# Optimization experiments

Hardware: AMD Instinct MI355X
Metric: run time of the kernel (lower is better)

## Reference

```python
import jax, jax.numpy as jnp
import numpy as np

TOP_K = 2
TEMP = 1.0  # router_temperature
B, L, D, F, DF, DR, DH, E = 32, 256, 256, 8, 64, 256, 512, 8
DIN = D + DF  # expert/router input: concat(hidden, feat_emb)


def setup_inputs() -> dict:
    key = jax.random.key(0)
    ks = jax.random.split(key, 12)
    gn = lambda k, shape, fan: jax.random.normal(k, shape, dtype=jnp.float32) * (fan ** -0.5)
    return {
        "hidden": jax.random.normal(ks[0], (B, L, D), dtype=jnp.float32),
        "feat": jax.random.uniform(ks[1], (B, L, F), dtype=jnp.float32),
        "W_feat": gn(ks[2], (F, DF), F),
        "b_feat": jnp.zeros((DF,), jnp.float32),
        "Wr1": gn(ks[3], (DIN, DR), DIN),
        "br1": jnp.zeros((DR,), jnp.float32),
        "Wr2": gn(ks[4], (DR, E), DR),
        "br2": jnp.zeros((E,), jnp.float32),
        "We1": gn(ks[5], (E, DIN, DH), DIN),
        "be1": jnp.zeros((E, DH), jnp.float32),
        "We2": gn(ks[6], (E, DH, D), DH),
        "be2": jnp.zeros((E, D), jnp.float32),
    }


def reference(hidden, feat, W_feat, b_feat, Wr1, br1, Wr2, br2, We1, be1, We2, be2):
    # feature embedding
    feat_emb = feat @ W_feat + b_feat                       # [B,L,DF]
    x = jnp.concatenate([hidden, feat_emb], axis=-1)        # [B,L,DIN]

    # token-level learned router with temperature + top-k gating
    hr = jax.nn.gelu(x @ Wr1 + br1)                         # [B,L,DR]
    gate_logits = (hr @ Wr2 + br2) / TEMP                   # [B,L,E]
    topv, topi = jax.lax.top_k(gate_logits, TOP_K)          # [B,L,K]
    w = jax.nn.softmax(topv, axis=-1)                       # renormalized over top-k
    gate_weights = (jax.nn.one_hot(topi, E, dtype=w.dtype) * w[..., None]).sum(-2)  # [B,L,E]

    # experts: per-expert 2-layer MLP (dense compute, sparse combine via gates)
    he = jax.nn.gelu(jnp.einsum('bli,eih->bleh', x, We1) + be1)   # [B,L,E,DH]
    eo = jnp.einsum('bleh,eho->bleo', he, We2) + be2              # [B,L,E,D]
    stage_delta = jnp.einsum('ble,bleo->blo', gate_weights, eo)   # next_hidden - hidden

    return stage_delta, gate_weights, gate_logits
```

## Files before the change

### kernel.cpp

```cpp
#include <hip/hip_runtime.h>
#include <hip/hip_bf16.h>

#define N_TOK   8192
#define DMODEL  256
#define NFEAT   8
#define DFEAT   64
#define DIN     320
#define DRTR    256
#define NE      8
#define DH      512
#define TE      32
#define RTB     32
#define FIXCAP  128
#define FIXTHR  2e-3f

#define OUT_GATEW  (N_TOK*DMODEL)
#define OUT_LOGITS (N_TOK*DMODEL + N_TOK*NE)

typedef short v8s __attribute__((ext_vector_type(8)));
typedef float v4f __attribute__((ext_vector_type(4)));

__device__ __forceinline__ unsigned short f2bf(float f){
  unsigned u = __float_as_uint(f);
  return (unsigned short)((u + 0x7FFFu + ((u>>16)&1u)) >> 16);
}
__device__ __forceinline__ float bf2f(unsigned short h){
  return __uint_as_float(((unsigned)h)<<16);
}
__device__ __forceinline__ float gelu_tanh(float v){
  float u = 0.7978845608028654f * (v + 0.044715f * v * v * v);
  float a = fabsf(u);
  float e = __expf(-2.0f * a);
  float t = (1.0f - e) / (1.0f + e);
  t = copysignf(t, u);
  return 0.5f * v * (1.0f + t);
}

__global__ __launch_bounds__(256) void k_prep(
    const float* __restrict__ We1, const float* __restrict__ We2,
    const float* __restrict__ Wr1,
    unsigned short* __restrict__ W1h, unsigned short* __restrict__ W1l,
    unsigned short* __restrict__ W2h, unsigned short* __restrict__ W2l,
    unsigned short* __restrict__ Wr1h, unsigned short* __restrict__ Wr1l,
    int* __restrict__ cnts, int* __restrict__ nfix)
{
  __shared__ float lds[16384];
  const int b = blockIdx.x;
  const int tid = threadIdx.x;
  if (b < 80){
    int e = b/10, kstep = b%10;
    const float* src = We1 + ((size_t)e*DIN + kstep*32)*DH;
    #pragma unroll
    for (int r=0;r<16;r++) ((float4*)lds)[r*256+tid] = ((const float4*)src)[r*256+tid];
    __syncthreads();
    #pragma unroll
    for (int r=0;r<8;r++){
      int ent = r*256+tid; int nt = ent>>6, l = ent&63;
      int n = nt*16 + (l&15); int k0 = (l>>4)*8;
      unsigned short hs[8], ls[8];
      #pragma unroll
      for (int i=0;i<8;i++){
        float v = lds[(k0+i)*DH + n];
        unsigned short h = f2bf(v);
        hs[i]=h; ls[i]=f2bf(v - bf2f(h));
      }
      size_t gid = ((size_t)(e*10+kstep)*32 + nt)*64 + l;
      *(v8s*)(W1h+gid*8) = *(v8s*)hs;
      *(v8s*)(W1l+gid*8) = *(v8s*)ls;
    }
  } else if (b < 208){
    int e = (b-80)/16, kstep = (b-80)%16;
    const float* src = We2 + ((size_t)e*DH + kstep*32)*DMODEL;
    #pragma unroll
    for (int r=0;r<8;r++) ((float4*)lds)[r*256+tid] = ((const float4*)src)[r*256+tid];
    __syncthreads();
    #pragma unroll
    for (int r=0;r<4;r++){
      int ent = r*256+tid; int nt = ent>>6, l = ent&63;
      int n = nt*16 + (l&15); int k0 = (l>>4)*8;
      unsigned short hs[8], ls[8];
      #pragma unroll
      for (int i=0;i<8;i++){
        float v = lds[(k0+i)*DMODEL + n];
        unsigned short h = f2bf(v);
        hs[i]=h; ls[i]=f2bf(v - bf2f(h));
      }
      size_t gid = ((size_t)(e*16+kstep)*16 + nt)*64 + l;
      *(v8s*)(W2h+gid*8) = *(v8s*)hs;
      *(v8s*)(W2l+gid*8) = *(v8s*)ls;
    }
  } else if (b < 218){
    int kstep = b-208;
    const float* src = Wr1 + (size_t)kstep*32*DRTR;
    #pragma unroll
    for (int r=0;r<8;r++) ((float4*)lds)[r*256+tid] = ((const float4*)src)[r*256+tid];
    __syncthreads();
    #pragma unroll
    for (int r=0;r<4;r++){
      int ent = r*256+tid; int nt = ent>>6, l = ent&63;
      int n = nt*16 + (l&15); int k0 = (l>>4)*8;
      unsigned short hs[8], ls[8];
      #pragma unroll
      for (int i=0;i<8;i++){
        float v = lds[(k0+i)*DRTR + n];
        unsigned short h = f2bf(v);
        hs[i]=h; ls[i]=f2bf(v - bf2f(h));
      }
      size_t gid = ((size_t)kstep*16 + nt)*64 + l;
      *(v8s*)(Wr1h+gid*8) = *(v8s*)hs;
      *(v8s*)(Wr1l+gid*8) = *(v8s*)ls;
    }
  } else {
    if (tid < NE) cnts[tid] = 0;
    if (tid == NE) *nfix = 0;
  }
}

#define MM6(c0,c1,ah0,ah1,al0,al1,bh,bl) do{ \
  c0 = __builtin_amdgcn_mfma_f32_16x16x32_bf16(ah0, bh, c0, 0,0,0); \
  c1 = __builtin_amdgcn_mfma_f32_16x16x32_bf16(ah1, bh, c1, 0,0,0); \
  c0 = __builtin_amdgcn_mfma_f32_16x16x32_bf16(al0, bh, c0, 0,0,0); \
  c1 = __builtin_amdgcn_mfma_f32_16x16x32_bf16(al1, bh, c1, 0,0,0); \
  c0 = __builtin_amdgcn_mfma_f32_16x16x32_bf16(ah0, bl, c0, 0,0,0); \
  c1 = __builtin_amdgcn_mfma_f32_16x16x32_bf16(ah1, bl, c1, 0,0,0); }while(0)

#define XLOFF  10496

__global__ __launch_bounds__(512) void k_rmfma(
    const float* __restrict__ hidden, const float* __restrict__ feat,
    const float* __restrict__ Wf, const float* __restrict__ bfe,
    const unsigned short* __restrict__ Wr1h, const unsigned short* __restrict__ Wr1l,
    const float* __restrict__ br1,
    const float* __restrict__ Wr2, const float* __restrict__ br2,
    float* __restrict__ out,
    int* __restrict__ cnts, unsigned* __restrict__ lists, float* __restrict__ topw,
    int* __restrict__ nfix, int* __restrict__ fixlist)
{
  __shared__ unsigned short sm[21248];
  __shared__ float part_lds[512];
  __shared__ float lg_lds[RTB*NE];
  float* hrf = (float*)sm;
  const int tid = threadIdx.x;
  const int t0 = blockIdx.x * RTB;

  {
    float4 z = make_float4(0.f,0.f,0.f,0.f);
    float4* dst = ((float4*)out) + (size_t)blockIdx.x*2048 + tid;
    #pragma unroll
    for (int r=0;r<4;r++) dst[r*512] = z;
  }
  #pragma unroll
  for (int r=0;r<4;r++){
    int idx = r*512 + tid; int t = idx >> 6, lane = idx & 63;
    float4 h4 = ((const float4*)(hidden + (size_t)(t0+t)*DMODEL))[lane];
    unsigned short h0=f2bf(h4.x),h1=f2bf(h4.y),h2=f2bf(h4.z),h3=f2bf(h4.w);
    unsigned short l0=f2bf(h4.x-bf2f(h0)),l1=f2bf(h4.y-bf2f(h1)),
                   l2=f2bf(h4.z-bf2f(h2)),l3=f2bf(h4.w-bf2f(h3));
    uint2 hp, lp;
    hp.x=(unsigned)h0|((unsigned)h1<<16); hp.y=(unsigned)h2|((unsigned)h3<<16);
    lp.x=(unsigned)l0|((unsigned)l1<<16); lp.y=(unsigned)l2|((unsigned)l3<<16);
    *(uint2*)&sm[t*328 + lane*4]         = hp;
    *(uint2*)&sm[XLOFF + t*328 + lane*4] = lp;
  }
  #pragma unroll
  for (int r=0;r<4;r++){
    int idx = r*512 + tid; int t = idx >> 6, j = idx & 63;
    float acc = bfe[j];
    #pragma unroll
    for (int f=0; f<NFEAT; f++) acc += feat[(size_t)(t0+t)*NFEAT + f] * Wf[f*DFEAT + j];
    unsigned short h = f2bf(acc);
    sm[t*328 + DMODEL + j]         = h;
    sm[XLOFF + t*328 + DMODEL + j] = f2bf(acc - bf2f(h));
  }
  __syncthreads();

  const int wv = tid >> 6;
  const int l  = tid & 63;
  const int lg = l >> 4;
  const int lr = l & 15;

  v4f acc[2][2];
  {
    v4f z = {0.f,0.f,0.f,0.f};
    acc[0][0]=z; acc[0][1]=z; acc[1][0]=z; acc[1][1]=z;
    v8s bh_a[2], bl_a[2], bh_b[2], bl_b[2];
    auto ldBr = [&](int ks, v8s (&bh)[2], v8s (&bl)[2]){
      #pragma unroll
      for (int j=0;j<2;++j){
        size_t boff = ((size_t)(ks*16 + wv*2 + j)*64 + l)*8;
        bh[j] = *(const v8s*)(Wr1h + boff);
        bl[j] = *(const v8s*)(Wr1l + boff);
      }
    };
    ldBr(0, bh_a, bl_a);
    for (int ks=0; ks<10; ks+=2){
      v8s ah0 = *(const v8s*)&sm[( 0+lr)*328 + ks*32 + lg*8];
      v8s ah1 = *(const v8s*)&sm[(16+lr)*328 + ks*32 + lg*8];
      v8s al0 = *(const v8s*)&sm[XLOFF + ( 0+lr)*328 + ks*32 + lg*8];
      v8s al1 = *(const v8s*)&sm[XLOFF + (16+lr)*328 + ks*32 + lg*8];
      ldBr(ks+1, bh_b, bl_b);
      __builtin_amdgcn_sched_barrier(0);
      #pragma unroll
      for (int j=0;j<2;++j) MM6(acc[0][j],acc[1][j], ah0,ah1,al0,al1, bh_a[j],bl_a[j]);
      v8s ch0 = *(const v8s*)&sm[( 0+lr)*328 + (ks+1)*32 + lg*8];
      v8s ch1 = *(const v8s*)&sm[(16+lr)*328 + (ks+1)*32 + lg*8];
      v8s cl0 = *(const v8s*)&sm[XLOFF + ( 0+lr)*328 + (ks+1)*32 + lg*8];
      v8s cl1 = *(const v8s*)&sm[XLOFF + (16+lr)*328 + (ks+1)*32 + lg*8];
      if (ks+2<10) ldBr(ks+2, bh_a, bl_a);
      __builtin_amdgcn_sched_barrier(0);
      #pragma unroll
      for (int j=0;j<2;++j) MM6(acc[0][j],acc[1][j], ch0,ch1,cl0,cl1, bh_b[j],bl_b[j]);
    }
  }
  __syncthreads();
  #pragma unroll
  for (int j=0;j<2;++j){
    int col = (wv*2+j)*16 + lr;
    float b1 = br1[col];
    #pragma unroll
    for (int m=0;m<2;m++)
      #pragma unroll
      for (int r=0;r<4;r++){
        int row = m*16 + lg*4 + r;
        hrf[row*264 + col] = gelu_tanh(acc[m][j][r] + b1);
      }
  }
  __syncthreads();
  {
    int q = tid >> 8, rr = tid & 255, t = rr >> 3, e = rr & 7;
    float a0=0.f,a1=0.f,a2=0.f,a3=0.f;
    #pragma unroll 4
    for (int k4=0;k4<32;k4++){
      float4 h4 = ((const float4*)hrf)[t*66 + q*32 + k4];
      int row = q*128 + k4*4;
      a0 += h4.x * Wr2[(row+0)*NE + e];
      a1 += h4.y * Wr2[(row+1)*NE + e];
      a2 += h4.z * Wr2[(row+2)*NE + e];
      a3 += h4.w * Wr2[(row+3)*NE + e];
    }
    part_lds[tid] = (a0+a1)+(a2+a3);
  }
  __syncthreads();
  if (tid < RTB*NE){
    int t = tid >> 3, e = tid & 7;
    float lgv = br2[e] + part_lds[tid] + part_lds[tid+256];
    out[OUT_LOGITS + (size_t)(t0+t)*NE + e] = lgv;
    lg_lds[t*NE + e] = lgv;
  }
  __syncthreads();
  if (tid < RTB){
    int t = tid, tok = t0 + t;
    float v1=-3.4e38f, v2=-3.4e38f, v3=-3.4e38f; int i1=-1, i2=-1;
    #pragma unroll
    for (int e=0;e<NE;e++){
      float v = lg_lds[t*NE+e];
      if (v > v1){ v3=v2; v2=v1; i2=i1; v1=v; i1=e; }
      else if (v > v2){ v3=v2; v2=v; i2=e; }
      else if (v > v3){ v3=v; }
    }
    bool defer = false;
    if (v2 - v3 < FIXTHR){
      int fi = atomicAdd(nfix, 1);
      if (fi < FIXCAP){ fixlist[fi] = tok; defer = true; }
    }
    if (!defer){
      float d   = expf(v2 - v1);
      float inv = 1.0f/(1.0f + d);
      float w1 = inv, w2 = d*inv;
      #pragma unroll
      for (int e=0;e<NE;e++){
        float gv = (e==i1) ? w1 : ((e==i2) ? w2 : 0.f);
        out[OUT_GATEW + (size_t)tok*NE + e] = gv;
      }
      int p1 = atomicAdd(&cnts[i1], 1);
      lists[i1*N_TOK + p1] = (unsigned)(tok<<1);
      int p2 = atomicAdd(&cnts[i2], 1);
      lists[i2*N_TOK + p2] = (unsigned)((tok<<1) | 1);
      topw[tok*2]   = w1;
      topw[tok*2+1] = w2;
    }
  }
}

__global__ __launch_bounds__(256) void k_fix(
    const float* __restrict__ hidden, const float* __restrict__ feat,
    const float* __restrict__ Wf, const float* __restrict__ bfe,
    const float* __restrict__ Wr1, const float* __restrict__ br1,
    const float* __restrict__ Wr2, const float* __restrict__ br2,
    float* __restrict__ out, const int* __restrict__ nfix, const int* __restrict__ fixlist)
{
  int nf = *nfix; if (nf > FIXCAP) nf = FIXCAP;
  if ((int)blockIdx.x >= nf) return;
  const int tok = fixlist[blockIdx.x];
  const int tid = threadIdx.x;
  __shared__ float xf[DIN];
  __shared__ float hr[DRTR];
  if (tid < DMODEL) xf[tid] = hidden[(size_t)tok*DMODEL + tid];
  if (tid < DFEAT){
    float acc = bfe[tid];
    #pragma unroll
    for (int f=0; f<NFEAT; f++) acc += feat[(size_t)tok*NFEAT + f] * Wf[f*DFEAT + tid];
    xf[DMODEL + tid] = acc;
  }
  __syncthreads();
  {
    float acc = br1[tid];
    for (int i=0;i<DIN;i++) acc += xf[i] * Wr1[(size_t)i*DRTR + tid];
    hr[tid] = gelu_tanh(acc);
  }
  __syncthreads();
  if (tid < NE){
    float acc = br2[tid];
    for (int i=0;i<DRTR;i++) acc += hr[i] * Wr2[i*NE + tid];
    out[OUT_LOGITS + (size_t)tok*NE + tid] = acc;
  }
}

__global__ void k_gatefix(float* __restrict__ out,
                          int* __restrict__ cnts, unsigned* __restrict__ lists,
                          float* __restrict__ topw,
                          const int* __restrict__ nfix, const int* __restrict__ fixlist)
{
  int nf = *nfix; if (nf > FIXCAP) nf = FIXCAP;
  int i = threadIdx.x;
  if (i >= nf) return;
  int tok = fixlist[i];
  float v1=-3.4e38f, v2=-3.4e38f; int i1=-1, i2=-1;
  #pragma unroll
  for (int e=0;e<NE;e++){
    float v = out[OUT_LOGITS + (size_t)tok*NE + e];
    if (v > v1){ v2=v1; i2=i1; v1=v; i1=e; }
    else if (v > v2){ v2=v; i2=e; }
  }
  float d   = expf(v2 - v1);
  float inv = 1.0f/(1.0f + d);
  float w1 = inv, w2 = d*inv;
  #pragma unroll
  for (int e=0;e<NE;e++){
    float gv = (e==i1) ? w1 : ((e==i2) ? w2 : 0.f);
    out[OUT_GATEW + (size_t)tok*NE + e] = gv;
  }
  int p1 = atomicAdd(&cnts[i1], 1);
  lists[i1*N_TOK + p1] = (unsigned)(tok<<1);
  int p2 = atomicAdd(&cnts[i2], 1);
  lists[i2*N_TOK + p2] = (unsigned)((tok<<1) | 1);
  topw[tok*2]   = w1;
  topw[tok*2+1] = w2;
}

#define XFL  10240
#define HFL  16384
__global__ __launch_bounds__(512) void k_expert(
    const float* __restrict__ hidden, const float* __restrict__ feat,
    const float* __restrict__ Wf, const float* __restrict__ bfe,
    const int* __restrict__ cnts, const unsigned* __restrict__ lists,
    const float* __restrict__ topw,
    const unsigned short* __restrict__ W1h, const unsigned short* __restrict__ W1l,
    const unsigned short* __restrict__ W2h, const unsigned short* __restrict__ W2l,
    const float* __restrict__ be1, const float* __restrict__ be2,
    float* __restrict__ out)
{
  __shared__ unsigned short sm[32768];
  __shared__ int   tok_lds[TE];
  __shared__ float w_lds[TE];

  const int e    = blockIdx.x & 7;
  const int tile = blockIdx.x >> 3;
  const int cnt  = cnts[e];
  const int start = tile * TE;
  if (start >= cnt) return;
  const int ntk = min(TE, cnt - start);
  const int tid = threadIdx.x;
  const int wv = tid >> 6;
  const int l  = tid & 63;
  const int lg = l >> 4;
  const int lr = l & 15;

  const unsigned short* p1h = W1h + (size_t)e*163840;
  const unsigned short* p1l = W1l + (size_t)e*163840;

  v8s bh_a[2], bl_a[2], bh_b[2], bl_b[2];
  auto ldB1 = [&](int ks, int jh, v8s (&bh)[2], v8s (&bl)[2]){
    #pragma unroll
    for (int j=0;j<2;++j){
      size_t boff = ((size_t)(ks*32 + wv*4 + jh*2 + j)*64 + l)*8;
      bh[j] = *(const v8s*)(p1h + boff);
      bl[j] = *(const v8s*)(p1l + boff);
    }
  };
  ldB1(0,0,bh_a,bl_a);

  if (tid < TE){
    if (tid < ntk){
      unsigned ent = lists[e*N_TOK + start + tid];
      int tok = (int)(ent >> 1);
      tok_lds[tid] = tok;
      w_lds[tid]   = topw[tok*2 + (ent & 1)];
    } else { tok_lds[tid] = -1; w_lds[tid] = 0.f; }
  }
  __syncthreads();
  #pragma unroll
  for (int r=0;r<3;r++){
    int idx = r*512 + tid;
    if (idx < 1280){
      int le = idx & 63; int rest = idx >> 6;
      int m = rest & 1, ks = rest >> 1;
      int t = m*16 + (le & 15);
      int kb = ks*32 + (le >> 4)*8;
      int tok = tok_lds[t];
      float v[8];
      if (tok < 0){
        #pragma unroll
        for (int i=0;i<8;i++) v[i] = 0.f;
      } else if (kb < DMODEL){
        float4 a = *(const float4*)(hidden + (size_t)tok*DMODEL + kb);
        float4 b = *(const float4*)(hidden + (size_t)tok*DMODEL + kb + 4);
        v[0]=a.x; v[1]=a.y; v[2]=a.z; v[3]=a.w;
        v[4]=b.x; v[5]=b.y; v[6]=b.z; v[7]=b.w;
      } else {
        int j0 = kb - DMODEL;
        #pragma unroll
        for (int i=0;i<8;i++){
          float acc = bfe[j0+i];
          #pragma unroll
          for (int f=0; f<NFEAT; f++) acc += feat[(size_t)tok*NFEAT + f] * Wf[f*DFEAT + j0+i];
          v[i] = acc;
        }
      }
      unsigned short hs[8], ls[8];
      #pragma unroll
      for (int i=0;i<8;i++){
        unsigned short h = f2bf(v[i]);
        hs[i]=h; ls[i]=f2bf(v[i]-bf2f(h));
      }
      *(v8s*)&sm[idx*8]       = *(v8s*)hs;
      *(v8s*)&sm[XFL + idx*8] = *(v8s*)ls;
    }
  }
  __syncthreads();

  v4f acc1[2][4];
  {
    v4f z = {0.f,0.f,0.f,0.f};
    #pragma unroll
    for (int m=0;m<2;m++)
      #pragma unroll
      for (int j=0;j<4;j++) acc1[m][j] = z;
    for (int ks=0; ks<10; ++ks){
      v8s ah0 = *(const v8s*)&sm[((ks*2+0)*64 + l)*8];
      v8s ah1 = *(const v8s*)&sm[((ks*2+1)*64 + l)*8];
      v8s al0 = *(const v8s*)&sm[XFL + ((ks*2+0)*64 + l)*8];
      v8s al1 = *(const v8s*)&sm[XFL + ((ks*2+1)*64 + l)*8];
      ldB1(ks,1,bh_b,bl_b);
      __builtin_amdgcn_sched_barrier(0);
      #pragma unroll
      for (int j=0;j<2;++j) MM6(acc1[0][j],acc1[1][j], ah0,ah1,al0,al1, bh_a[j],bl_a[j]);
      if (ks<9) ldB1(ks+1,0,bh_a,bl_a);
      __builtin_amdgcn_sched_barrier(0);
      #pragma unroll
      for (int j=0;j<2;++j) MM6(acc1[0][2+j],acc1[1][2+j], ah0,ah1,al0,al1, bh_b[j],bl_b[j]);
    }
  }
  const unsigned short* p2h = W2h + (size_t)e*131072;
  const unsigned short* p2l = W2l + (size_t)e*131072;
  v8s ch_a[2], cl_a[2], ch_b[2], cl_b[2];
  auto ldB2 = [&](int ks, v8s (&bh)[2], v8s (&bl)[2]){
    #pragma unroll
    for (int j=0;j<2;++j){
      size_t boff = ((size_t)(ks*16 + wv*2 + j)*64 + l)*8;
      bh[j] = *(const v8s*)(p2h + boff);
      bl[j] = *(const v8s*)(p2l + boff);
    }
  };
  ldB2(0, ch_a, cl_a);
  __syncthreads();
  #pragma unroll
  for (int j=0;j<4;++j){
    int W = wv*4 + j;
    int col = W*16 + lr;
    float b1 = be1[e*DH + col];
    int ks2 = W >> 1;
    int lg2 = (W*2 + (lr>>3)) & 3;
    int i   = lr & 7;
    #pragma unroll
    for (int m=0;m<2;m++)
      #pragma unroll
      for (int r=0;r<4;r++){
        float v = gelu_tanh(acc1[m][j][r] + b1);
        unsigned short h = f2bf(v);
        int dst = ((ks2*2 + m)*64 + lg2*16 + lg*4 + r)*8 + i;
        sm[dst]       = h;
        sm[HFL + dst] = f2bf(v - bf2f(h));
      }
  }
  __syncthreads();
  v4f acc2[2][2];
  {
    v4f z = {0.f,0.f,0.f,0.f};
    acc2[0][0]=z; acc2[0][1]=z; acc2[1][0]=z; acc2[1][1]=z;
    for (int ks=0; ks<16; ks+=2){
      v8s ah0 = *(const v8s*)&sm[((ks*2+0)*64 + l)*8];
      v8s ah1 = *(const v8s*)&sm[((ks*2+1)*64 + l)*8];
      v8s al0 = *(const v8s*)&sm[HFL + ((ks*2+0)*64 + l)*8];
      v8s al1 = *(const v8s*)&sm[HFL + ((ks*2+1)*64 + l)*8];
      ldB2(ks+1, ch_b, cl_b);
      __builtin_amdgcn_sched_barrier(0);
      #pragma unroll
      for (int j=0;j<2;++j) MM6(acc2[0][j],acc2[1][j], ah0,ah1,al0,al1, ch_a[j],cl_a[j]);
      v8s dh0 = *(const v8s*)&sm[(((ks+1)*2+0)*64 + l)*8];
      v8s dh1 = *(const v8s*)&sm[(((ks+1)*2+1)*64 + l)*8];
      v8s dl0 = *(const v8s*)&sm[HFL + (((ks+1)*2+0)*64 + l)*8];
      v8s dl1 = *(const v8s*)&sm[HFL + (((ks+1)*2+1)*64 + l)*8];
      if (ks+2<16) ldB2(ks+2, ch_a, cl_a);
      __builtin_amdgcn_sched_barrier(0);
      #pragma unroll
      for (int j=0;j<2;++j) MM6(acc2[0][j],acc2[1][j], dh0,dh1,dl0,dl1, ch_b[j],cl_b[j]);
    }
  }
  #pragma unroll
  for (int j=0;j<2;++j){
    int col = (wv*2+j)*16 + lr;
    float b2 = be2[e*DMODEL + col];
    #pragma unroll
    for (int m=0;m<2;m++)
      #pragma unroll
      for (int r=0;r<4;r++){
        int row = m*16 + lg*4 + r;
        if (row < ntk){
          float w = w_lds[row];
          atomicAdd(out + (size_t)tok_lds[row]*DMODEL + col,
                    w*(acc2[m][j][r] + b2));
        }
      }
  }
}

extern "C" void kernel_launch(void* const* d_in, const int* in_sizes, int n_in,
                              void* d_out, int out_size, void* d_ws, size_t ws_size,
                              hipStream_t stream)
{
  (void)in_sizes; (void)n_in; (void)out_size; (void)ws_size;
  const float* hidden = (const float*)d_in[0];
  const float* feat   = (const float*)d_in[1];
  const float* Wf     = (const float*)d_in[2];
  const float* bfe    = (const float*)d_in[3];
  const float* Wr1    = (const float*)d_in[4];
  const float* br1    = (const float*)d_in[5];
  const float* Wr2    = (const float*)d_in[6];
  const float* br2    = (const float*)d_in[7];
  const float* We1    = (const float*)d_in[8];
  const float* be1    = (const float*)d_in[9];
  const float* We2    = (const float*)d_in[10];
  const float* be2    = (const float*)d_in[11];
  float* out = (float*)d_out;

  char* ws = (char*)d_ws;
  int*      cnts    = (int*)ws;
  int*      nfix    = (int*)(ws + 64);
  int*      fixlist = (int*)(ws + 128);
  unsigned* lists   = (unsigned*)(ws + 1024);
  float*    topw    = (float*)(ws + 263168);
  unsigned short* W1h  = (unsigned short*)(ws + 328704);
  unsigned short* W1l  = (unsigned short*)(ws + 2950144);
  unsigned short* W2h  = (unsigned short*)(ws + 5571584);
  unsigned short* W2l  = (unsigned short*)(ws + 7668736);
  unsigned short* Wr1h = (unsigned short*)(ws + 9765888);
  unsigned short* Wr1l = (unsigned short*)(ws + 9929728);

  hipLaunchKernelGGL(k_prep, dim3(219), dim3(256), 0, stream,
                     We1, We2, Wr1, W1h, W1l, W2h, W2l, Wr1h, Wr1l, cnts, nfix);
  hipLaunchKernelGGL(k_rmfma, dim3(N_TOK/RTB), dim3(512), 0, stream,
                     hidden, feat, Wf, bfe, Wr1h, Wr1l, br1, Wr2, br2,
                     out, cnts, lists, topw, nfix, fixlist);
  hipLaunchKernelGGL(k_fix, dim3(FIXCAP), dim3(256), 0, stream,
                     hidden, feat, Wf, bfe, Wr1, br1, Wr2, br2, out, nfix, fixlist);
  hipLaunchKernelGGL(k_gatefix, dim3(1), dim3(FIXCAP), 0, stream,
                     out, cnts, lists, topw, nfix, fixlist);
  hipLaunchKernelGGL(k_expert, dim3((N_TOK/TE)*NE), dim3(512), 0, stream,
                     hidden, feat, Wf, bfe, cnts, lists, topw,
                     W1h, W1l, W2h, W2l, be1, be2, out);
}
```

Baseline: 310.3 us.

## Halve router token tile, reorder expert grid by expert, drop sched barriers

The router kernel now processes 16 tokens per block instead of 32. Its MFMA loop uses a single 16-row A tile with a new 3-product split-bf16 macro, and the Wr2 reduction is split four ways. This doubles the number of router blocks and reuses each Wr1 load over fewer tokens. The expert kernel's block index is reordered so that consecutive blocks share the same expert, which should improve L2 reuse of expert weights, and the sched_barrier hints in its MFMA loops are removed.

```diff
diff --git a/kernel.cpp b/kernel.cpp
--- a/kernel.cpp
+++ b/kernel.cpp
@@ -10,7 +10,7 @@
 #define NE      8
 #define DH      512
 #define TE      32
-#define RTB     32
+#define RTB     16
 #define FIXCAP  128
 #define FIXTHR  2e-3f
 
@@ -123,8 +123,12 @@
   c1 = __builtin_amdgcn_mfma_f32_16x16x32_bf16(al1, bh, c1, 0,0,0); \
   c0 = __builtin_amdgcn_mfma_f32_16x16x32_bf16(ah0, bl, c0, 0,0,0); \
   c1 = __builtin_amdgcn_mfma_f32_16x16x32_bf16(ah1, bl, c1, 0,0,0); }while(0)
-
-#define XLOFF  10496
+#define MM3(c0,ah0,al0,bh,bl) do{ \
+  c0 = __builtin_amdgcn_mfma_f32_16x16x32_bf16(ah0, bh, c0, 0,0,0); \
+  c0 = __builtin_amdgcn_mfma_f32_16x16x32_bf16(al0, bh, c0, 0,0,0); \
+  c0 = __builtin_amdgcn_mfma_f32_16x16x32_bf16(ah0, bl, c0, 0,0,0); }while(0)
+
+#define XLOFF  5248
 
 __global__ __launch_bounds__(512) void k_rmfma(
     const float* __restrict__ hidden, const float* __restrict__ feat,
@@ -136,7 +140,7 @@
     int* __restrict__ cnts, unsigned* __restrict__ lists, float* __restrict__ topw,
     int* __restrict__ nfix, int* __restrict__ fixlist)
 {
-  __shared__ unsigned short sm[21248];
+  __shared__ unsigned short sm[10496];
   __shared__ float part_lds[512];
   __shared__ float lg_lds[RTB*NE];
   float* hrf = (float*)sm;
@@ -145,12 +149,11 @@
 
   {
     float4 z = make_float4(0.f,0.f,0.f,0.f);
-    float4* dst = ((float4*)out) + (size_t)blockIdx.x*2048 + tid;
-    #pragma unroll
-    for (int r=0;r<4;r++) dst[r*512] = z;
-  }
-  #pragma unroll
-  for (int r=0;r<4;r++){
+    float4* dst = ((float4*)out) + (size_t)blockIdx.x*1024 + tid;
+    dst[0] = z; dst[512] = z;
+  }
+  #pragma unroll
+  for (int r=0;r<2;r++){
     int idx = r*512 + tid; int t = idx >> 6, lane = idx & 63;
     float4 h4 = ((const float4*)(hidden + (size_t)(t0+t)*DMODEL))[lane];
     unsigned short h0=f2bf(h4.x),h1=f2bf(h4.y),h2=f2bf(h4.z),h3=f2bf(h4.w);
@@ -163,7 +166,7 @@
     *(uint2*)&sm[XLOFF + t*328 + lane*4] = lp;
   }
   #pragma unroll
-  for (int r=0;r<4;r++){
+  for (int r=0;r<2;r++){
     int idx = r*512 + tid; int t = idx >> 6, j = idx & 63;
     float acc = bfe[j];
     #pragma unroll
@@ -179,10 +182,10 @@
   const int lg = l >> 4;
   const int lr = l & 15;
 
-  v4f acc[2][2];
+  v4f acc[2];
   {
     v4f z = {0.f,0.f,0.f,0.f};
-    acc[0][0]=z; acc[0][1]=z; acc[1][0]=z; acc[1][1]=z;
+    acc[0]=z; acc[1]=z;
     v8s bh_a[2], bl_a[2], bh_b[2], bl_b[2];
     auto ldBr = [&](int ks, v8s (&bh)[2], v8s (&bl)[2]){
       #pragma unroll
@@ -194,22 +197,16 @@
     };
     ldBr(0, bh_a, bl_a);
     for (int ks=0; ks<10; ks+=2){
-      v8s ah0 = *(const v8s*)&sm[( 0+lr)*328 + ks*32 + lg*8];
-      v8s ah1 = *(const v8s*)&sm[(16+lr)*328 + ks*32 + lg*8];
-      v8s al0 = *(const v8s*)&sm[XLOFF + ( 0+lr)*328 + ks*32 + lg*8];
-      v8s al1 = *(const v8s*)&sm[XLOFF + (16+lr)*328 + ks*32 + lg*8];
+      v8s ah0 = *(const v8s*)&sm[lr*328 + ks*32 + lg*8];
+      v8s al0 = *(const v8s*)&sm[XLOFF + lr*328 + ks*32 + lg*8];
       ldBr(ks+1, bh_b, bl_b);
-      __builtin_amdgcn_sched_barrier(0);
-      #pragma unroll
-      for (int j=0;j<2;++j) MM6(acc[0][j],acc[1][j], ah0,ah1,al0,al1, bh_a[j],bl_a[j]);
-      v8s ch0 = *(const v8s*)&sm[( 0+lr)*328 + (ks+1)*32 + lg*8];
-      v8s ch1 = *(const v8s*)&sm[(16+lr)*328 + (ks+1)*32 + lg*8];
-      v8s cl0 = *(const v8s*)&sm[XLOFF + ( 0+lr)*328 + (ks+1)*32 + lg*8];
-      v8s cl1 = *(const v8s*)&sm[XLOFF + (16+lr)*328 + (ks+1)*32 + lg*8];
+      #pragma unroll
+      for (int j=0;j<2;++j) MM3(acc[j], ah0,al0, bh_a[j],bl_a[j]);
+      v8s ch0 = *(const v8s*)&sm[lr*328 + (ks+1)*32 + lg*8];
+      v8s cl0 = *(const v8s*)&sm[XLOFF + lr*328 + (ks+1)*32 + lg*8];
       if (ks+2<10) ldBr(ks+2, bh_a, bl_a);
-      __builtin_amdgcn_sched_barrier(0);
-      #pragma unroll
-      for (int j=0;j<2;++j) MM6(acc[0][j],acc[1][j], ch0,ch1,cl0,cl1, bh_b[j],bl_b[j]);
+      #pragma unroll
+      for (int j=0;j<2;++j) MM3(acc[j], ch0,cl0, bh_b[j],bl_b[j]);
     }
   }
   __syncthreads();
@@ -218,21 +215,19 @@
     int col = (wv*2+j)*16 + lr;
     float b1 = br1[col];
     #pragma unroll
-    for (int m=0;m<2;m++)
-      #pragma unroll
-      for (int r=0;r<4;r++){
-        int row = m*16 + lg*4 + r;
-        hrf[row*264 + col] = gelu_tanh(acc[m][j][r] + b1);
-      }
+    for (int r=0;r<4;r++){
+      int row = lg*4 + r;
+      hrf[row*264 + col] = gelu_tanh(acc[j][r] + b1);
+    }
   }
   __syncthreads();
   {
-    int q = tid >> 8, rr = tid & 255, t = rr >> 3, e = rr & 7;
+    int q = tid >> 7, rr = tid & 127, t = rr >> 3, e = rr & 7;
     float a0=0.f,a1=0.f,a2=0.f,a3=0.f;
     #pragma unroll 4
-    for (int k4=0;k4<32;k4++){
-      float4 h4 = ((const float4*)hrf)[t*66 + q*32 + k4];
-      int row = q*128 + k4*4;
+    for (int k4=0;k4<16;k4++){
+      float4 h4 = ((const float4*)hrf)[t*66 + q*16 + k4];
+      int row = q*64 + k4*4;
       a0 += h4.x * Wr2[(row+0)*NE + e];
       a1 += h4.y * Wr2[(row+1)*NE + e];
       a2 += h4.z * Wr2[(row+2)*NE + e];
@@ -243,7 +238,7 @@
   __syncthreads();
   if (tid < RTB*NE){
     int t = tid >> 3, e = tid & 7;
-    float lgv = br2[e] + part_lds[tid] + part_lds[tid+256];
+    float lgv = br2[e] + part_lds[tid] + part_lds[tid+128] + part_lds[tid+256] + part_lds[tid+384];
     out[OUT_LOGITS + (size_t)(t0+t)*NE + e] = lgv;
     lg_lds[t*NE + e] = lgv;
   }
@@ -364,8 +359,8 @@
   __shared__ int   tok_lds[TE];
   __shared__ float w_lds[TE];
 
-  const int e    = blockIdx.x & 7;
-  const int tile = blockIdx.x >> 3;
+  const int e    = blockIdx.x >> 8;
+  const int tile = blockIdx.x & 255;
   const int cnt  = cnts[e];
   const int start = tile * TE;
   if (start >= cnt) return;
@@ -452,11 +447,9 @@
       v8s al0 = *(const v8s*)&sm[XFL + ((ks*2+0)*64 + l)*8];
       v8s al1 = *(const v8s*)&sm[XFL + ((ks*2+1)*64 + l)*8];
       ldB1(ks,1,bh_b,bl_b);
-      __builtin_amdgcn_sched_barrier(0);
       #pragma unroll
       for (int j=0;j<2;++j) MM6(acc1[0][j],acc1[1][j], ah0,ah1,al0,al1, bh_a[j],bl_a[j]);
       if (ks<9) ldB1(ks+1,0,bh_a,bl_a);
-      __builtin_amdgcn_sched_barrier(0);
       #pragma unroll
       for (int j=0;j<2;++j) MM6(acc1[0][2+j],acc1[1][2+j], ah0,ah1,al0,al1, bh_b[j],bl_b[j]);
     }
@@ -504,7 +497,6 @@
       v8s al0 = *(const v8s*)&sm[HFL + ((ks*2+0)*64 + l)*8];
       v8s al1 = *(const v8s*)&sm[HFL + ((ks*2+1)*64 + l)*8];
       ldB2(ks+1, ch_b, cl_b);
-      __builtin_amdgcn_sched_barrier(0);
       #pragma unroll
       for (int j=0;j<2;++j) MM6(acc2[0][j],acc2[1][j], ah0,ah1,al0,al1, ch_a[j],cl_a[j]);
       v8s dh0 = *(const v8s*)&sm[(((ks+1)*2+0)*64 + l)*8];
@@ -512,7 +504,6 @@
       v8s dl0 = *(const v8s*)&sm[HFL + (((ks+1)*2+0)*64 + l)*8];
       v8s dl1 = *(const v8s*)&sm[HFL + (((ks+1)*2+1)*64 + l)*8];
       if (ks+2<16) ldB2(ks+2, ch_a, cl_a);
-      __builtin_amdgcn_sched_barrier(0);
       #pragma unroll
       for (int j=0;j<2;++j) MM6(acc2[0][j],acc2[1][j], dh0,dh1,dl0,dl1, ch_b[j],cl_b[j]);
     }
@@ -576,7 +567,7 @@
                      hidden, feat, Wf, bfe, Wr1, br1, Wr2, br2, out, nfix, fixlist);
   hipLaunchKernelGGL(k_gatefix, dim3(1), dim3(FIXCAP), 0, stream,
                      out, cnts, lists, topw, nfix, fixlist);
-  hipLaunchKernelGGL(k_expert, dim3((N_TOK/TE)*NE), dim3(512), 0, stream,
+  hipLaunchKernelGGL(k_expert, dim3(NE*256), dim3(512), 0, stream,
                      hidden, feat, Wf, bfe, cnts, lists, topw,
                      W1h, W1l, W2h, W2l, be1, be2, out);
 }
```

Result: faster. 270.1 us (-13.0%).
